# Optimization experiments

Hardware: AMD Instinct MI355X
Metric: run time of the kernel (lower is better)

## Reference

```python
import jax, jax.numpy as jnp
import numpy as np

NUM_HEADS = 16
D_MODEL = 1024
BATCH = 4
SEQ = 1024


def setup_inputs() -> dict:
    key = jax.random.key(0)
    k_x, k_m, k_wqkv, k_bqkv, k_wo, k_bo = jax.random.split(key, 6)
    d = D_MODEL
    scale = 1.0 / np.sqrt(d)
    return {
        "x": jax.random.normal(k_x, (BATCH, SEQ, d), dtype=jnp.float32),
        "mask": jax.random.randint(k_m, (BATCH, SEQ, SEQ), 0, 2, dtype=jnp.int32),
        "Wqkv": jax.random.normal(k_wqkv, (d, 3 * d), dtype=jnp.float32) * scale,
        "bqkv": jax.random.normal(k_bqkv, (3 * d,), dtype=jnp.float32) * 0.02,
        "Wo": jax.random.normal(k_wo, (d, d), dtype=jnp.float32) * scale,
        "bo": jax.random.normal(k_bo, (d,), dtype=jnp.float32) * 0.02,
    }


def reference(x, mask, Wqkv, bqkv, Wo, bo):
    B, S, D = x.shape
    H = NUM_HEADS
    hd = D // H
    # fused QKV projection: [B,S,3D] -> [B,S,H,3*hd] -> [B,H,S,3*hd]
    qkv = (x @ Wqkv + bqkv).reshape(B, S, H, 3 * hd).transpose(0, 2, 1, 3)
    q, k, v = jnp.split(qkv, 3, axis=-1)  # each [B,H,S,hd]
    # scores [B,H,S,S], scaled by sqrt(head_dim)
    scores = jnp.einsum("bhqd,bhkd->bhqk", q, k) / jnp.sqrt(jnp.float32(hd))
    scores = jnp.where(mask[:, None, :, :] == 0, jnp.float32(-1e20), scores)
    attn = jax.nn.softmax(scores, axis=-1)
    vals = jnp.einsum("bhqk,bhkd->bhqd", attn, v)  # [B,H,S,hd]
    vals = vals.transpose(0, 2, 1, 3).reshape(B, S, D)
    return vals @ Wo + bo
```

## Files before the change

### kernel.cpp

```cpp
#include <hip/hip_runtime.h>
#include <cstddef>
#include <cstdint>

#define BATCH 4
#define SEQ   1024
#define DM    1024
#define NH    16
#define HD    64
#define D3    3072
#define LOG2E 1.44269504088896340736f
#define QSCALE (0.125f * LOG2E)

typedef _Float16 f16x8 __attribute__((ext_vector_type(8)));
typedef _Float16 f16x4 __attribute__((ext_vector_type(4)));
typedef __fp16   h16x2 __attribute__((ext_vector_type(2)));
typedef float    f32x4 __attribute__((ext_vector_type(4)));

#define MFMA16(a, b, c) __builtin_amdgcn_mfma_f32_16x16x32_f16((a), (b), (c), 0, 0, 0)
#define GLD_LDS16(gp, lp) \
  __builtin_amdgcn_global_load_lds((const __attribute__((address_space(1))) unsigned int*)(gp), \
                                   (__attribute__((address_space(3))) unsigned int*)(lp), 16, 0, 0)
#if __has_builtin(__builtin_amdgcn_exp2f)
#define EXP2(x) __builtin_amdgcn_exp2f(x)
#else
#define EXP2(x) exp2f(x)
#endif

__global__ __launch_bounds__(256) void prep(const float* __restrict__ x,
                                            _Float16* __restrict__ x16,
                                            const int* __restrict__ mask,
                                            unsigned long long* __restrict__ mb) {
  const int tid = threadIdx.x;
  if (blockIdx.x < 2048) {
    const int i = blockIdx.x * 256 + tid;
    float4 a = ((const float4*)x)[i * 2];
    float4 b = ((const float4*)x)[i * 2 + 1];
    f16x8 o;
    o[0] = (_Float16)a.x; o[1] = (_Float16)a.y; o[2] = (_Float16)a.z; o[3] = (_Float16)a.w;
    o[4] = (_Float16)b.x; o[5] = (_Float16)b.y; o[6] = (_Float16)b.z; o[7] = (_Float16)b.w;
    ((f16x8*)x16)[i] = o;
  } else {
    const size_t i = (size_t)(blockIdx.x - 2048) * 256 + tid;
    const int m = mask[i];
    unsigned long long bits = __ballot(m != 0);
    if ((tid & 63) == 0) mb[i >> 6] = bits;
  }
}

__global__ __launch_bounds__(256) void transpose_cast2(const float* __restrict__ W1,
                                                       _Float16* __restrict__ WT1,
                                                       const float* __restrict__ W2,
                                                       _Float16* __restrict__ WT2) {
  __shared__ _Float16 T[64 * 72];
  const int tid = threadIdx.x;
  const bool first = blockIdx.x < 48;
  const float* W = first ? W1 : W2;
  _Float16* WT = first ? WT1 : WT2;
  const int N = first ? D3 : DM;
  const int K = DM;
  const int c0 = (first ? blockIdx.x : (blockIdx.x - 48)) * 64;
  const int r0 = blockIdx.y * 64;
#pragma unroll
  for (int it = 0; it < 4; ++it) {
    const int row = it * 16 + (tid >> 4);
    const int col4 = (tid & 15) * 4;
    float4 wv = *(const float4*)(W + (size_t)(r0 + row) * N + c0 + col4);
    T[(col4 + 0) * 72 + row] = (_Float16)wv.x;
    T[(col4 + 1) * 72 + row] = (_Float16)wv.y;
    T[(col4 + 2) * 72 + row] = (_Float16)wv.z;
    T[(col4 + 3) * 72 + row] = (_Float16)wv.w;
  }
  __syncthreads();
#pragma unroll
  for (int it = 0; it < 2; ++it) {
    const int g = it * 256 + tid;
    const int col = g >> 3, seg = g & 7;
    *(f16x8*)(WT + (size_t)(c0 + col) * K + r0 + seg * 8) = *(const f16x8*)(T + col * 72 + seg * 8);
  }
}

template <typename OutT, bool QKV, int TN>
__global__ __launch_bounds__(256) void gemm_bt(const _Float16* __restrict__ A,
                                               const _Float16* __restrict__ BT,
                                               const float* __restrict__ bias,
                                               OutT* __restrict__ C,
                                               _Float16* __restrict__ vTp,
                                               int M, int N, int K) {
  constexpr int NT = TN / 32;
  __shared__ _Float16 As[128 * 64];
  __shared__ _Float16 Bs[TN * 64];
  const int tid = threadIdx.x;
  const int l15 = tid & 15;
  const int quad = (tid & 63) >> 4;
  const int w = tid >> 6;
  const int wm = w >> 1, wn = w & 1;
  const int rowbase = blockIdx.y * 128;
  const int colbase = blockIdx.x * TN;

  f32x4 acc[4][NT];
#pragma unroll
  for (int mt = 0; mt < 4; ++mt)
#pragma unroll
    for (int nt = 0; nt < NT; ++nt) acc[mt][nt] = (f32x4){0.f, 0.f, 0.f, 0.f};

  for (int k0 = 0; k0 < K; k0 += 64) {
    __syncthreads();
#pragma unroll
    for (int it = 0; it < 4; ++it) {
      const int g = it * 256 + tid;
      const int r = g >> 3, cs = (g & 7) ^ (r & 7);
      GLD_LDS16(A + (size_t)(rowbase + r) * K + k0 + cs * 8, As + g * 8);
    }
#pragma unroll
    for (int it = 0; it < TN / 32; ++it) {
      const int g = it * 256 + tid;
      const int r = g >> 3, cs = (g & 7) ^ (r & 7);
      GLD_LDS16(BT + (size_t)(colbase + r) * K + k0 + cs * 8, Bs + g * 8);
    }
    __syncthreads();
#pragma unroll
    for (int kh = 0; kh < 2; ++kh) {
      f16x8 a[4], b[NT];
#pragma unroll
      for (int mt = 0; mt < 4; ++mt) {
        const int row = wm * 64 + mt * 16 + l15;
        a[mt] = *(const f16x8*)(As + row * 64 + (((kh * 4 + quad) ^ (row & 7)) << 3));
      }
#pragma unroll
      for (int nt = 0; nt < NT; ++nt) {
        const int row = wn * (TN / 2) + nt * 16 + l15;
        b[nt] = *(const f16x8*)(Bs + row * 64 + (((kh * 4 + quad) ^ (row & 7)) << 3));
      }
#pragma unroll
      for (int mt = 0; mt < 4; ++mt)
#pragma unroll
        for (int nt = 0; nt < NT; ++nt)
          acc[mt][nt] = MFMA16(a[mt], b[nt], acc[mt][nt]);
    }
  }

  float bv[NT];
#pragma unroll
  for (int nt = 0; nt < NT; ++nt) bv[nt] = bias[colbase + wn * (TN / 2) + nt * 16 + l15];
#pragma unroll
  for (int mt = 0; mt < 4; ++mt)
#pragma unroll
    for (int nt = 0; nt < NT; ++nt) {
      const int col = colbase + wn * (TN / 2) + nt * 16 + l15;
      if (QKV) {
        const int reg3 = (col >> 6) % 3;
        if (reg3 == 2) {
          const int hh = col / 192;
          const int d = col - hh * 192 - 128;
          const int row0 = rowbase + wm * 64 + mt * 16 + quad * 4;
          const int bb = row0 >> 10, s0 = row0 & 1023;
          f16x4 pk;
#pragma unroll
          for (int r = 0; r < 4; ++r) pk[r] = (_Float16)(acc[mt][nt][r] + bv[nt]);
          *(f16x4*)(vTp + ((size_t)((bb * NH + hh) * HD + d)) * SEQ + s0) = pk;
        } else {
          const float sc = (reg3 == 0) ? QSCALE : 1.f;
#pragma unroll
          for (int r = 0; r < 4; ++r) {
            const int row = rowbase + wm * 64 + mt * 16 + quad * 4 + r;
            C[(size_t)row * N + col] = (OutT)((acc[mt][nt][r] + bv[nt]) * sc);
          }
        }
      } else {
#pragma unroll
        for (int r = 0; r < 4; ++r) {
          const int row = rowbase + wm * 64 + mt * 16 + quad * 4 + r;
          C[(size_t)row * N + col] = (OutT)(acc[mt][nt][r] + bv[nt]);
        }
      }
    }
}

__global__ __launch_bounds__(256) void attn(const _Float16* __restrict__ qkv,
                                            const _Float16* __restrict__ vT,
                                            const unsigned long long* __restrict__ mb,
                                            _Float16* __restrict__ vals) {
  __shared__ _Float16 Ks[64 * 72];
  __shared__ _Float16 Vt[64 * 72];
  __shared__ _Float16 Ps[4][32 * 72];
  __shared__ __align__(8) _Float16 LUT[16][4];
  const int tid = threadIdx.x;
  const int l15 = tid & 15, quad = (tid & 63) >> 4, w = tid >> 6;
  const int i = blockIdx.x;
  const int bh = (i >> 6) * 8 + (i & 7);
  const int b = bh >> 4, h = bh & 15;
  const int q0 = ((i >> 3) & 7) << 7;

  if (tid < 16) {
    LUT[tid][0] = (tid & 1) ? (_Float16)1.f : (_Float16)0.f;
    LUT[tid][1] = (tid & 2) ? (_Float16)1.f : (_Float16)0.f;
    LUT[tid][2] = (tid & 4) ? (_Float16)1.f : (_Float16)0.f;
    LUT[tid][3] = (tid & 8) ? (_Float16)1.f : (_Float16)0.f;
  }

  const _Float16* qb = qkv + (size_t)b * SEQ * D3 + h * 192;
  f16x8 qf[2][2];
#pragma unroll
  for (int qn = 0; qn < 2; ++qn)
#pragma unroll
    for (int hf = 0; hf < 2; ++hf)
      qf[qn][hf] = *(const f16x8*)(qb + (size_t)(q0 + w * 32 + qn * 16 + l15) * D3 +
                                   hf * 32 + quad * 8);

  const _Float16* kg = qb + 64;
  const _Float16* vg = vT + (size_t)((b * NH + h) * HD) * SEQ;
  const int sr = tid >> 3, sseg = tid & 7;
  const int vd = tid >> 2, vs = tid & 3;
  const size_t mb0 = (size_t)(b * SEQ + q0 + w * 32 + l15) * 16;
  const size_t mb1 = (size_t)(b * SEQ + q0 + w * 32 + 16 + l15) * 16;

  f16x8 k0r = *(const f16x8*)(kg + (size_t)sr * D3 + sseg * 8);
  f16x8 k1r = *(const f16x8*)(kg + (size_t)(sr + 32) * D3 + sseg * 8);
  f16x8 v0r = *(const f16x8*)(vg + (size_t)vd * SEQ + vs * 8);
  f16x8 v1r = *(const f16x8*)(vg + (size_t)vd * SEQ + 32 + vs * 8);
  unsigned long long mr0 = mb[mb0], mr1 = mb[mb1];

  f32x4 lacc[2];
  f32x4 o_[2][4];
#pragma unroll
  for (int qn = 0; qn < 2; ++qn) {
    lacc[qn] = (f32x4){0.f, 0.f, 0.f, 0.f};
#pragma unroll
    for (int dt = 0; dt < 4; ++dt) o_[qn][dt] = (f32x4){0.f, 0.f, 0.f, 0.f};
  }
  f16x8 ones;
#pragma unroll
  for (int i2 = 0; i2 < 8; ++i2) ones[i2] = (_Float16)1.f;

  for (int kt = 0; kt < 16; ++kt) {
    if (kt) __syncthreads();
    *(f16x8*)(Ks + sr * 72 + sseg * 8) = k0r;
    *(f16x8*)(Ks + (sr + 32) * 72 + sseg * 8) = k1r;
    *(f16x8*)(Vt + vd * 72 + vs * 8) = v0r;
    *(f16x8*)(Vt + vd * 72 + 32 + vs * 8) = v1r;
    __syncthreads();
    const unsigned long long mc[2] = {mr0, mr1};
    if (kt < 15) {
      const int kn = (kt + 1) << 6;
      k0r = *(const f16x8*)(kg + (size_t)(kn + sr) * D3 + sseg * 8);
      k1r = *(const f16x8*)(kg + (size_t)(kn + sr + 32) * D3 + sseg * 8);
      v0r = *(const f16x8*)(vg + (size_t)vd * SEQ + kn + vs * 8);
      v1r = *(const f16x8*)(vg + (size_t)vd * SEQ + kn + 32 + vs * 8);
      mr0 = mb[mb0 + kt + 1];
      mr1 = mb[mb1 + kt + 1];
    }
    f32x4 st[4][2];
#pragma unroll
    for (int mt = 0; mt < 4; ++mt)
#pragma unroll
      for (int qn = 0; qn < 2; ++qn) st[mt][qn] = (f32x4){0.f, 0.f, 0.f, 0.f};
#pragma unroll
    for (int mt = 0; mt < 4; ++mt) {
      f16x8 ka0 = *(const f16x8*)(Ks + (mt * 16 + l15) * 72 + quad * 8);
      f16x8 ka1 = *(const f16x8*)(Ks + (mt * 16 + l15) * 72 + 32 + quad * 8);
#pragma unroll
      for (int qn = 0; qn < 2; ++qn) {
        st[mt][qn] = MFMA16(ka0, qf[qn][0], st[mt][qn]);
        st[mt][qn] = MFMA16(ka1, qf[qn][1], st[mt][qn]);
      }
    }
#pragma unroll
    for (int qn = 0; qn < 2; ++qn)
#pragma unroll
      for (int mt = 0; mt < 4; ++mt) {
        float e0 = EXP2(fminf(st[mt][qn][0], 15.f));
        float e1 = EXP2(fminf(st[mt][qn][1], 15.f));
        float e2 = EXP2(fminf(st[mt][qn][2], 15.f));
        float e3 = EXP2(fminf(st[mt][qn][3], 15.f));
        h16x2 lo = __builtin_amdgcn_cvt_pkrtz(e0, e1);
        h16x2 hi = __builtin_amdgcn_cvt_pkrtz(e2, e3);
        f16x4 pk;
        pk[0] = (_Float16)lo[0]; pk[1] = (_Float16)lo[1];
        pk[2] = (_Float16)hi[0]; pk[3] = (_Float16)hi[1];
        const unsigned nib = (unsigned)(mc[qn] >> (mt * 16 + quad * 4)) & 15u;
        pk *= *(const f16x4*)LUT[nib];
        *(f16x4*)(&Ps[w][(qn * 16 + l15) * 72 + mt * 16 + quad * 4]) = pk;
      }
    f16x8 pa[2][2];
#pragma unroll
    for (int qn = 0; qn < 2; ++qn) {
      pa[qn][0] = *(const f16x8*)(&Ps[w][(qn * 16 + l15) * 72 + quad * 8]);
      pa[qn][1] = *(const f16x8*)(&Ps[w][(qn * 16 + l15) * 72 + 32 + quad * 8]);
      lacc[qn] = MFMA16(pa[qn][0], ones, lacc[qn]);
      lacc[qn] = MFMA16(pa[qn][1], ones, lacc[qn]);
    }
#pragma unroll
    for (int dt = 0; dt < 4; ++dt) {
      f16x8 vb0 = *(const f16x8*)(Vt + (dt * 16 + l15) * 72 + quad * 8);
      f16x8 vb1 = *(const f16x8*)(Vt + (dt * 16 + l15) * 72 + 32 + quad * 8);
#pragma unroll
      for (int qn = 0; qn < 2; ++qn) {
        o_[qn][dt] = MFMA16(pa[qn][0], vb0, o_[qn][dt]);
        o_[qn][dt] = MFMA16(pa[qn][1], vb1, o_[qn][dt]);
      }
    }
  }
#pragma unroll
  for (int qn = 0; qn < 2; ++qn) {
    f32x4 inv;
#pragma unroll
    for (int r = 0; r < 4; ++r) inv[r] = 1.f / lacc[qn][r];
#pragma unroll
    for (int dt = 0; dt < 4; ++dt)
#pragma unroll
      for (int r = 0; r < 4; ++r)
        vals[(size_t)(b * SEQ + q0 + w * 32 + qn * 16 + quad * 4 + r) * DM +
             h * HD + dt * 16 + l15] = (_Float16)(o_[qn][dt][r] * inv[r]);
  }
}

extern "C" void kernel_launch(void* const* d_in, const int* in_sizes, int n_in,
                              void* d_out, int out_size, void* d_ws, size_t ws_size,
                              hipStream_t stream) {
  const float* x    = (const float*)d_in[0];
  const int*   mask = (const int*)  d_in[1];
  const float* Wqkv = (const float*)d_in[2];
  const float* bqkv = (const float*)d_in[3];
  const float* Wo   = (const float*)d_in[4];
  const float* bo   = (const float*)d_in[5];
  float* out = (float*)d_out;

  char* ws = (char*)d_ws;
  _Float16* qkv16  = (_Float16*)ws;                    ws += (size_t)BATCH*SEQ*D3*2;
  _Float16* vT16   = (_Float16*)ws;                    ws += (size_t)BATCH*DM*SEQ*2;
  _Float16* x16    = (_Float16*)ws;                    ws += (size_t)BATCH*SEQ*DM*2;
  _Float16* WqkvT  = (_Float16*)ws;                    ws += (size_t)DM*D3*2;
  _Float16* WoT    = (_Float16*)ws;                    ws += (size_t)DM*DM*2;
  _Float16* vals16 = (_Float16*)ws;                    ws += (size_t)BATCH*SEQ*DM*2;
  unsigned long long* mbits = (unsigned long long*)ws;

  prep<<<2048 + (BATCH*SEQ*SEQ)/256, 256, 0, stream>>>(x, x16, mask, mbits);
  transpose_cast2<<<dim3(64, 16), 256, 0, stream>>>(Wqkv, WqkvT, Wo, WoT);

  gemm_bt<_Float16, true, 128><<<dim3(D3/128, BATCH*SEQ/128), 256, 0, stream>>>(
      x16, WqkvT, bqkv, qkv16, vT16, BATCH*SEQ, D3, DM);
  attn<<<512, 256, 0, stream>>>(qkv16, vT16, mbits, vals16);
  gemm_bt<float, false, 64><<<dim3(DM/64, (BATCH*SEQ)/128), 256, 0, stream>>>(
      vals16, WoT, bo, out, nullptr, BATCH*SEQ, DM, DM);
}
```

Before: 191.7 us.

## Replace QKV projection GEMM with 256x256-tile 8-wave pipelined kernel

After: 190.0 us. About the same (-0.9%).

```diff
diff --git a/kernel.cpp b/kernel.cpp
--- a/kernel.cpp
+++ b/kernel.cpp
@@ -176,6 +176,150 @@
     }
 }
 
+#define BAR() asm volatile("s_barrier" ::: "memory")
+#define WVM(N) asm volatile("s_waitcnt vmcnt(" #N ")" ::: "memory")
+
+#define LDAF(BUF, KK)                                                           \
+  _Pragma("unroll") for (int mt = 0; mt < 8; ++mt) {                            \
+    const int rr = wm * 128 + mt * 16 + l15;                                    \
+    const int idx = ((rr >> 1) << 3) |                                          \
+                    ((((rr & 1) << 2) | quad) ^ ((rr >> 1) & 7));               \
+    af[mt] = *(const f16x8*)(&LA[BUF][(KK) * 8192 + idx * 8]);                  \
+  }
+
+#define LDBF(BUF, KK, NQ)                                                       \
+  _Pragma("unroll") for (int t = 0; t < 2; ++t) {                               \
+    const int rr = wn * 64 + (NQ) * 32 + t * 16 + l15;                          \
+    const int idx = ((rr >> 1) << 3) |                                          \
+                    ((((rr & 1) << 2) | quad) ^ ((rr >> 1) & 7));               \
+    bf[t] = *(const f16x8*)(&LB[BUF][(KK) * 8192 + idx * 8]);                   \
+  }
+
+#define MFMAQ(NQ)                                                               \
+  __builtin_amdgcn_s_setprio(1);                                                \
+  _Pragma("unroll") for (int mt = 0; mt < 8; ++mt) {                            \
+    acc[mt][(NQ) * 2 + 0] = MFMA16(af[mt], bf[0], acc[mt][(NQ) * 2 + 0]);       \
+    acc[mt][(NQ) * 2 + 1] = MFMA16(af[mt], bf[1], acc[mt][(NQ) * 2 + 1]);       \
+  }                                                                             \
+  __builtin_amdgcn_s_setprio(0);
+
+__global__ __launch_bounds__(512, 2) void gemm_qkv8(const _Float16* __restrict__ A,
+                                                    const _Float16* __restrict__ BT,
+                                                    const float* __restrict__ bias,
+                                                    _Float16* __restrict__ C,
+                                                    _Float16* __restrict__ vTp) {
+  __shared__ __align__(16) _Float16 LA[2][2 * 8192];
+  __shared__ __align__(16) _Float16 LB[2][2 * 8192];
+  const int tid = threadIdx.x;
+  const int l15 = tid & 15, quad = (tid & 63) >> 4, w = tid >> 6;
+  const int wm = w >> 2, wn = w & 3;
+  const int rowbase = blockIdx.y * 256, colbase = blockIdx.x * 256;
+
+  f32x4 acc[8][4];
+#pragma unroll
+  for (int mt = 0; mt < 8; ++mt)
+#pragma unroll
+    for (int nt = 0; nt < 4; ++nt) acc[mt][nt] = (f32x4){0.f, 0.f, 0.f, 0.f};
+
+  auto stage = [&](const _Float16* __restrict__ G, int tb, int kt, int h,
+                   _Float16* Lr) {
+#pragma unroll
+    for (int it2 = 0; it2 < 2; ++it2) {
+      const int g = it2 * 512 + tid;
+      const int pr = g >> 3, s = g & 7;
+      const int inv = s ^ (pr & 7);
+      const int r2 = (pr << 1) | (inv >> 2), c = inv & 3;
+      GLD_LDS16(G + (size_t)(tb + r2) * DM + (kt << 6) + (h << 5) + (c << 3),
+                Lr + g * 8);
+    }
+  };
+
+  stage(A, rowbase, 0, 0, &LA[0][0]);
+  stage(BT, colbase, 0, 0, &LB[0][0]);
+  stage(A, rowbase, 0, 1, &LA[0][8192]);
+  stage(BT, colbase, 0, 1, &LB[0][8192]);
+  stage(A, rowbase, 1, 0, &LA[1][0]);
+  stage(BT, colbase, 1, 0, &LB[1][0]);
+  WVM(8);
+  BAR();
+
+#pragma unroll 1
+  for (int it = 0; it < 7; ++it) {
+    const int t1 = 2 * it + 1, t2 = 2 * it + 2, t3 = 2 * it + 3;
+    f16x8 af[8], bf[2];
+    LDAF(0, 0) LDBF(0, 0, 0) stage(A, rowbase, t1, 1, &LA[1][8192]);
+    BAR(); MFMAQ(0) BAR();
+    LDBF(0, 0, 1) stage(BT, colbase, t1, 1, &LB[1][8192]);
+    BAR(); MFMAQ(1) WVM(8); BAR();
+    LDAF(0, 1) LDBF(0, 1, 0) stage(A, rowbase, t2, 0, &LA[0][0]);
+    BAR(); MFMAQ(0) BAR();
+    LDBF(0, 1, 1) stage(BT, colbase, t2, 0, &LB[0][0]);
+    BAR(); MFMAQ(1) WVM(8); BAR();
+    LDAF(1, 0) LDBF(1, 0, 0) stage(A, rowbase, t2, 1, &LA[0][8192]);
+    BAR(); MFMAQ(0) BAR();
+    LDBF(1, 0, 1) stage(BT, colbase, t2, 1, &LB[0][8192]);
+    BAR(); MFMAQ(1) WVM(8); BAR();
+    LDAF(1, 1) LDBF(1, 1, 0) stage(A, rowbase, t3, 0, &LA[1][0]);
+    BAR(); MFMAQ(0) BAR();
+    LDBF(1, 1, 1) stage(BT, colbase, t3, 0, &LB[1][0]);
+    BAR(); MFMAQ(1) WVM(8); BAR();
+  }
+  {
+    f16x8 af[8], bf[2];
+    LDAF(0, 0) LDBF(0, 0, 0) stage(A, rowbase, 15, 1, &LA[1][8192]);
+    BAR(); MFMAQ(0) BAR();
+    LDBF(0, 0, 1) stage(BT, colbase, 15, 1, &LB[1][8192]);
+    BAR(); MFMAQ(1) WVM(8); BAR();
+    LDAF(0, 1) LDBF(0, 1, 0)
+    BAR(); MFMAQ(0) BAR();
+    LDBF(0, 1, 1)
+    BAR(); MFMAQ(1) WVM(4); BAR();
+    LDAF(1, 0) LDBF(1, 0, 0)
+    BAR(); MFMAQ(0) BAR();
+    LDBF(1, 0, 1)
+    BAR(); MFMAQ(1) WVM(0); BAR();
+    LDAF(1, 1) LDBF(1, 1, 0)
+    BAR(); MFMAQ(0) BAR();
+    LDBF(1, 1, 1)
+    BAR(); MFMAQ(1) BAR();
+  }
+
+  float bv[4];
+#pragma unroll
+  for (int nt = 0; nt < 4; ++nt) bv[nt] = bias[colbase + wn * 64 + nt * 16 + l15];
+  const int cb6 = (colbase >> 6) + wn;
+  const int r3 = cb6 % 3;
+  if (r3 == 2) {
+    const int hh = cb6 / 3;
+#pragma unroll
+    for (int mt = 0; mt < 8; ++mt) {
+      const int row0 = rowbase + wm * 128 + mt * 16 + quad * 4;
+      const int bb = row0 >> 10, s0 = row0 & 1023;
+#pragma unroll
+      for (int nt = 0; nt < 4; ++nt) {
+        const int d = colbase + wn * 64 + nt * 16 + l15 - hh * 192 - 128;
+        f16x4 pk;
+#pragma unroll
+        for (int r = 0; r < 4; ++r) pk[r] = (_Float16)(acc[mt][nt][r] + bv[nt]);
+        *(f16x4*)(vTp + ((size_t)((bb * NH + hh) * HD + d)) * SEQ + s0) = pk;
+      }
+    }
+  } else {
+    const float sc = (r3 == 0) ? QSCALE : 1.f;
+#pragma unroll
+    for (int mt = 0; mt < 8; ++mt) {
+      const int row0 = rowbase + wm * 128 + mt * 16 + quad * 4;
+#pragma unroll
+      for (int nt = 0; nt < 4; ++nt) {
+        const int col = colbase + wn * 64 + nt * 16 + l15;
+#pragma unroll
+        for (int r = 0; r < 4; ++r)
+          C[(size_t)(row0 + r) * D3 + col] = (_Float16)((acc[mt][nt][r] + bv[nt]) * sc);
+      }
+    }
+  }
+}
+
 __global__ __launch_bounds__(256) void attn(const _Float16* __restrict__ qkv,
                                             const _Float16* __restrict__ vT,
                                             const unsigned long long* __restrict__ mb,
@@ -337,8 +481,8 @@
   prep<<<2048 + (BATCH*SEQ*SEQ)/256, 256, 0, stream>>>(x, x16, mask, mbits);
   transpose_cast2<<<dim3(64, 16), 256, 0, stream>>>(Wqkv, WqkvT, Wo, WoT);
 
-  gemm_bt<_Float16, true, 128><<<dim3(D3/128, BATCH*SEQ/128), 256, 0, stream>>>(
-      x16, WqkvT, bqkv, qkv16, vT16, BATCH*SEQ, D3, DM);
+  gemm_qkv8<<<dim3(D3/256, BATCH*SEQ/256), 512, 0, stream>>>(
+      x16, WqkvT, bqkv, qkv16, vT16);
   attn<<<512, 256, 0, stream>>>(qkv16, vT16, mbits, vals16);
   gemm_bt<float, false, 64><<<dim3(DM/64, (BATCH*SEQ)/128), 256, 0, stream>>>(
       vals16, WoT, bo, out, nullptr, BATCH*SEQ, DM, DM);
```
